# Kernel tuning notes

Measured on AMD Instinct MI355X. Metric: run time of the kernel, lower is better.

Reference implementation:

```python
import jax, jax.numpy as jnp
import numpy as np

INPUT_DIM = 1024
OUTPUT_DIM = 1024
NUM_SEGMENTS = 8
GRID_LO, GRID_HI = -1.0, 1.0


def setup_inputs() -> dict:
    key = jax.random.key(0)
    k1, k2 = jax.random.split(key)
    x = jax.random.normal(k1, (8, 2048, INPUT_DIM), dtype=jnp.float32)
    coeff = jax.random.normal(k2, (NUM_SEGMENTS + 1, OUTPUT_DIM, INPUT_DIM), dtype=jnp.float32) * 0.1
    bias = jnp.zeros((OUTPUT_DIM,), dtype=jnp.float32)
    return {"x": x, "coeff": coeff, "bias": bias}


def reference(x, coeff, bias):
    # x: (..., I); coeff: (G, O, I) with G = num_segments + 1; bias: (O,)
    batch_shape = x.shape[:-1]
    x_flat = x.reshape(-1, INPUT_DIM)                      # (B, I)
    grid = jnp.linspace(GRID_LO, GRID_HI, NUM_SEGMENTS + 1, dtype=x.dtype)  # (G,)
    h = (GRID_HI - GRID_LO) / NUM_SEGMENTS

    x_mean = jnp.mean(x_flat, axis=-1, keepdims=True)      # (B, 1)
    diff = x_mean - grid[None, :]                          # (B, G)
    w = jax.nn.relu(1.0 - jnp.abs(diff) / h)               # triangular hat weights
    w = w / (jnp.sum(w, axis=-1, keepdims=True) + 1e-8)    # (B, G)

    # Fused contraction order: avoid the (B, O, I) intermediate of the
    # original einsum chain; same math by associativity.
    t = jnp.einsum('bi,goi->bgo', x_flat, coeff)           # (B, G, O)
    out = jnp.einsum('bg,bgo->bo', w, t) + bias            # (B, O)
    return out.reshape(*batch_shape, OUTPUT_DIM)
```

## Files before the change

kernel.cpp:

```cpp
#include <hip/hip_runtime.h>
#include <math.h>

#define B_ROWS 16384
#define IDIM   1024
#define ODIM   1024
#define NGRID  9

#define RS_BLOCKS 1024
#define RS_ROWS   (B_ROWS / RS_BLOCKS)

#define GEMM_MSLOTS 80
#define GEMM_NT     8
#define GEMM_BLOCKS (GEMM_MSLOTS * GEMM_NT)

typedef __attribute__((ext_vector_type(8))) short frag8;
typedef __attribute__((ext_vector_type(4))) float f32x4;

typedef __attribute__((address_space(1))) void gvoid;
typedef __attribute__((address_space(3))) void lvoid;

__device__ __forceinline__ void async_cp16(const void* g, void* l) {
  __builtin_amdgcn_global_load_lds((gvoid*)(void*)g, (lvoid*)l, 16, 0, 0);
}

__device__ __forceinline__ unsigned short f2bf(float f) {
  union { float f; unsigned u; } v; v.f = f;
  unsigned u = v.u;
  u += 0x7fffu + ((u >> 16) & 1u);
  return (unsigned short)(u >> 16);
}

__device__ __forceinline__ void seg_weights(float m, int& sI, float& w0, float& w1) {
  float wsum = 0.f, wg[NGRID];
#pragma unroll
  for (int g = 0; g < NGRID; g++) {
    float gv = -1.f + 0.25f * (float)g;
    float t = 1.f - fabsf(m - gv) * 4.f;
    wg[g] = t > 0.f ? t : 0.f;
    wsum += wg[g];
  }
  int s = (int)floorf((m + 1.f) * 4.f);
  s = s < 0 ? 0 : (s > 7 ? 7 : s);
  float inv = 1.f / (wsum + 1e-8f);
  sI = s;
  w0 = wg[s] * inv;
  w1 = wg[s + 1] * inv;
}

__global__ void row_stats_fused(const float* __restrict__ x,
                                unsigned short* __restrict__ Xb,
                                float2* __restrict__ ws2,
                                int* __restrict__ seg_rows,
                                int* __restrict__ bucket_cnt) {
  __shared__ int lcnt[NGRID];
  __shared__ int base[NGRID];
  __shared__ int lrank[RS_ROWS];
  __shared__ int lseg[RS_ROWS];
  const int tid  = threadIdx.x;
  const int lane = tid & 63;
  const int wave = tid >> 6;
  if (tid < NGRID) lcnt[tid] = 0;
  __syncthreads();
  const int row0 = blockIdx.x * RS_ROWS;
#pragma unroll
  for (int it = 0; it < RS_ROWS / 4; ++it) {
    int r = it * 4 + wave;
    int b = row0 + r;
    const float4* xr = (const float4*)(x + (size_t)b * IDIM);
    ushort4* xw = (ushort4*)(Xb + (size_t)b * IDIM);
    float4 v[4];
    float s = 0.f;
#pragma unroll
    for (int j = 0; j < 4; j++) {
      v[j] = xr[lane + j * 64];
      s += v[j].x + v[j].y + v[j].z + v[j].w;
    }
#pragma unroll
    for (int j = 0; j < 4; j++) {
      ushort4 u;
      u.x = f2bf(v[j].x); u.y = f2bf(v[j].y); u.z = f2bf(v[j].z); u.w = f2bf(v[j].w);
      xw[lane + j * 64] = u;
    }
#pragma unroll
    for (int off = 32; off; off >>= 1) s += __shfl_down(s, off, 64);
    if (lane == 0) {
      float m = s * (1.0f / (float)IDIM);
      int sI; float w0, w1;
      seg_weights(m, sI, w0, w1);
      ws2[b] = make_float2(w0, w1);
      lseg[r] = sI;
      lrank[r] = atomicAdd(&lcnt[sI], 1);
    }
  }
  __syncthreads();
  if (tid < NGRID) base[tid] = lcnt[tid] ? atomicAdd(&bucket_cnt[tid], lcnt[tid]) : 0;
  __syncthreads();
  if (tid < RS_ROWS)
    seg_rows[lseg[tid] * B_ROWS + base[lseg[tid]] + lrank[tid]] = row0 + tid;
}

#define CV_BLKS_PER_PLANE (ODIM * IDIM / 4 / 256)
__global__ void cvt_coeff(const float* __restrict__ c, unsigned short* __restrict__ cb,
                          const int* __restrict__ bucket_cnt) {
  const int g  = blockIdx.x >> 10;
  const int cI = blockIdx.x & 1023;
  bool need = bucket_cnt[g] > 0;
  if (!need && g > 0) need = bucket_cnt[g - 1] > 0;
  if (!need) return;
  int i = (g * CV_BLKS_PER_PLANE + cI) * 256 + threadIdx.x;
  float4 v = ((const float4*)c)[i];
  ushort4 o;
  o.x = f2bf(v.x); o.y = f2bf(v.y); o.z = f2bf(v.z); o.w = f2bf(v.w);
  ((ushort4*)cb)[i] = o;
}

__global__ void __launch_bounds__(512, 2)
kan_gemm(const unsigned short* __restrict__ Xb,
         const unsigned short* __restrict__ Cb,
         const int* __restrict__ seg_rows,
         const int* __restrict__ bucket_cnt,
         const float2* __restrict__ ws2,
         const float* __restrict__ bias,
         float* __restrict__ out) {
  const int sub = blockIdx.x & 63;
  const int mt  = (blockIdx.x >> 6) * 8 + (sub & 7);
  const int nt  = sub >> 3;

  int seg = -1, lt = 0, cnt = 0;
  {
    int t0 = 0;
#pragma unroll
    for (int g = 0; g < NGRID; g++) {
      int c   = bucket_cnt[g];
      int ntg = (c + 255) >> 8;
      if (mt >= t0 && mt < t0 + ntg) { seg = g; lt = mt - t0; cnt = c; }
      t0 += ntg;
    }
  }
  if (seg < 0) return;
  const int rlim = cnt - lt * 256;
  const int* rows = seg_rows + seg * B_ROWS + lt * 256;

  __shared__ unsigned short As[2][256 * 64];
  __shared__ unsigned short Bs[2][256 * 64];
  __shared__ unsigned short scratch[512];

  const int tid  = threadIdx.x;
  const int lane = tid & 63;
  const int wave = tid >> 6;
  const int wm   = wave >> 2;
  const int wn   = wave & 3;
  const int colB0 = nt * 128;

  const int srow = lane >> 3;
  const int sc   = lane & 7;
  const int swc  = (((sc >> 2) ^ (srow & 1)) << 2) | ((sc & 3) ^ ((srow >> 1) & 3));
  const unsigned swkB = (unsigned)swc * 16;

  unsigned aOff[2][2], bOff[2][2];
#pragma unroll
  for (int h = 0; h < 2; h++)
#pragma unroll
    for (int i = 0; i < 2; i++) {
      int idx = h * 128 + wave * 16 + i * 8 + srow;
      int rid = rows[idx < rlim ? idx : rlim - 1];
      aOff[h][i] = (unsigned)rid * (IDIM * 2) + swkB;
      int realcol = wave * 16 + i * 8 + srow;
      bOff[h][i] = (unsigned)((seg + h) * ODIM + colB0 + realcol) * (IDIM * 2) + swkB;
    }

  int rofs[2];
#pragma unroll
  for (int kh = 0; kh < 2; kh++)
    rofs[kh] = ((((kh ^ (lane & 1)) << 2) | (((lane >> 4) & 3) ^ ((lane >> 1) & 3))) ) * 8;

  f32x4 acc[8][4] = {};
  frag8 af[8];
  frag8 bf[8];

#define STAGE_A(B, T, H) do {                                                  \
    const int tt_ = (T);                                                       \
    _Pragma("unroll")                                                          \
    for (int i_ = 0; i_ < 2; i_++) {                                           \
      unsigned short* dst_ = (tt_ < 16) ? &As[B][((H) * 128 + wave * 16 + i_ * 8) * 64] : scratch; \
      const char* src_ = (const char*)Xb + (tt_ < 16 ? (size_t)(aOff[H][i_] + (unsigned)tt_ * 128) : (size_t)swkB); \
      async_cp16(src_, dst_);                                                  \
    }                                                                          \
  } while (0)

#define STAGE_B(B, T, H) do {                                                  \
    const int tt_ = (T);                                                       \
    _Pragma("unroll")                                                          \
    for (int i_ = 0; i_ < 2; i_++) {                                           \
      unsigned short* dst_ = (tt_ < 16) ? &Bs[B][((H) * 128 + wave * 16 + i_ * 8) * 64] : scratch; \
      const char* src_ = (const char*)Cb + (tt_ < 16 ? (size_t)(bOff[H][i_] + (unsigned)tt_ * 128) : (size_t)swkB); \
      async_cp16(src_, dst_);                                                  \
    }                                                                          \
  } while (0)

#define LOAD_AF(B, MH) do {                                                    \
    _Pragma("unroll")                                                          \
    for (int mi_ = 0; mi_ < 4; mi_++)                                          \
      _Pragma("unroll")                                                        \
      for (int kh_ = 0; kh_ < 2; kh_++)                                        \
        af[mi_ * 2 + kh_] = *(const frag8*)&As[B][((MH) * 128 + wm * 64 + mi_ * 16 + (lane & 15)) * 64 + rofs[kh_]]; \
  } while (0)

#define LOAD_BF(B, NH) do {                                                    \
    _Pragma("unroll")                                                          \
    for (int ni_ = 0; ni_ < 2; ni_++)                                          \
      _Pragma("unroll")                                                        \
      for (int kh_ = 0; kh_ < 2; kh_++)                                        \
        bf[((NH) * 2 + ni_) * 2 + kh_] = *(const frag8*)&Bs[B][((NH) * 128 + wn * 32 + ni_ * 16 + (lane & 15)) * 64 + rofs[kh_]]; \
  } while (0)

#define MFMA_Q(MH, NH) do {                                                    \
    __builtin_amdgcn_s_setprio(1);                                             \
    _Pragma("unroll")                                                          \
    for (int mi_ = 0; mi_ < 4; mi_++)                                          \
      _Pragma("unroll")                                                        \
      for (int ni_ = 0; ni_ < 2; ni_++)                                        \
        _Pragma("unroll")                                                      \
        for (int kh_ = 0; kh_ < 2; kh_++)                                      \
          acc[(MH) * 4 + mi_][(NH) * 2 + ni_] = __builtin_amdgcn_mfma_f32_16x16x32_bf16( \
              af[mi_ * 2 + kh_], bf[((NH) * 2 + ni_) * 2 + kh_],               \
              acc[(MH) * 4 + mi_][(NH) * 2 + ni_], 0, 0, 0);                   \
    __builtin_amdgcn_s_setprio(0);                                             \
  } while (0)

#define VM10 asm volatile("s_waitcnt vmcnt(10)" ::: "memory")
#define BAR  asm volatile("s_barrier" ::: "memory")

  STAGE_A(0, 0, 0);
  STAGE_B(0, 0, 0);
  STAGE_B(0, 0, 1);
  STAGE_A(0, 0, 1);
  STAGE_A(1, 1, 0);
  STAGE_B(1, 1, 0);
  STAGE_B(1, 1, 1);
  VM10;
  BAR;

#pragma unroll 2
  for (int t = 0; t < 16; ++t) {
    const int buf  = t & 1;
    const int nbuf = buf ^ 1;
    LOAD_AF(buf, 0);
    LOAD_BF(buf, 0);
    STAGE_A(nbuf, t + 1, 1);
    VM10; BAR;
    MFMA_Q(0, 0);
    BAR;
    LOAD_BF(buf, 1);
    STAGE_A(buf, t + 2, 0);
    VM10; BAR;
    MFMA_Q(0, 1);
    BAR;
    LOAD_AF(buf, 1);
    STAGE_B(buf, t + 2, 0);
    BAR;
    MFMA_Q(1, 1);
    BAR;
    STAGE_B(buf, t + 2, 1);
    MFMA_Q(1, 0);
    VM10; BAR;
  }
#undef STAGE_A
#undef STAGE_B
#undef LOAD_AF
#undef LOAD_BF
#undef MFMA_Q

  int   col[2]; float bv[2];
#pragma unroll
  for (int nc = 0; nc < 2; nc++) {
    col[nc] = colB0 + wn * 32 + nc * 16 + (lane & 15);
    bv[nc]  = bias[col[nc]];
  }
#pragma unroll
  for (int mi = 0; mi < 8; mi++) {
    int irow = (mi >> 2) * 128 + wm * 64 + (mi & 3) * 16 + (lane >> 4) * 4;
#pragma unroll
    for (int r = 0; r < 4; r++) {
      int idx = irow + r;
      if (idx < rlim) {
        int orow = rows[idx];
        float2 w = ws2[orow];
        float* o = out + (size_t)orow * ODIM;
#pragma unroll
        for (int nc = 0; nc < 2; nc++)
          o[col[nc]] = w.x * acc[mi][nc][r] + w.y * acc[mi][2 + nc][r] + bv[nc];
      }
    }
  }
}

__global__ void fallback_kernel(const float* __restrict__ x, const float* __restrict__ coeff,
                                const float* __restrict__ bias, float* __restrict__ out) {
  int b = blockIdx.x;
  int tid = threadIdx.x;
  __shared__ float xs[IDIM];
  __shared__ float ps[4];
  __shared__ float mw[2];
  __shared__ int   ms;
  float4 v = ((const float4*)(x + (size_t)b * IDIM))[tid];
  ((float4*)xs)[tid] = v;
  float s = v.x + v.y + v.z + v.w;
#pragma unroll
  for (int off = 32; off; off >>= 1) s += __shfl_down(s, off, 64);
  if ((tid & 63) == 0) ps[tid >> 6] = s;
  __syncthreads();
  if (tid == 0) {
    float m = (ps[0] + ps[1] + ps[2] + ps[3]) * (1.0f / (float)IDIM);
    int sI; float w0, w1;
    seg_weights(m, sI, w0, w1);
    mw[0] = w0; mw[1] = w1; ms = sI;
  }
  __syncthreads();
  float w0 = mw[0], w1 = mw[1]; int sI = ms;
  for (int o = tid; o < ODIM; o += 256) {
    const float* c0 = coeff + ((size_t)sI * ODIM + o) * IDIM;
    const float* c1 = c0 + (size_t)ODIM * IDIM;
    float a0 = 0.f, a1 = 0.f;
    for (int i = 0; i < IDIM; i++) { a0 += xs[i] * c0[i]; a1 += xs[i] * c1[i]; }
    out[(size_t)b * ODIM + o] = w0 * a0 + w1 * a1 + bias[o];
  }
}

extern "C" void kernel_launch(void* const* d_in, const int* in_sizes, int n_in,
                              void* d_out, int out_size, void* d_ws, size_t ws_size,
                              hipStream_t stream) {
  const float* x     = (const float*)d_in[0];
  const float* coeff = (const float*)d_in[1];
  const float* bias  = (const float*)d_in[2];
  float* out = (float*)d_out;

  size_t szXb = (size_t)B_ROWS * IDIM * sizeof(unsigned short);
  size_t szCb = (size_t)NGRID * ODIM * IDIM * sizeof(unsigned short);
  size_t o0 = 0;
  unsigned short* Xb = (unsigned short*)((char*)d_ws + o0); o0 += szXb;
  unsigned short* Cb = (unsigned short*)((char*)d_ws + o0); o0 += szCb;
  float2* ws2 = (float2*)((char*)d_ws + o0); o0 += (size_t)B_ROWS * 8;
  int* seg_rows = (int*)((char*)d_ws + o0); o0 += (size_t)NGRID * B_ROWS * 4;
  int* bucket_cnt = (int*)((char*)d_ws + o0); o0 += 256;

  if (ws_size < o0) {
    fallback_kernel<<<B_ROWS, 256, 0, stream>>>(x, coeff, bias, out);
    return;
  }

  hipMemsetAsync(bucket_cnt, 0, NGRID * sizeof(int), stream);
  row_stats_fused<<<RS_BLOCKS, 256, 0, stream>>>(x, Xb, ws2, seg_rows, bucket_cnt);
  cvt_coeff<<<NGRID * CV_BLKS_PER_PLANE, 256, 0, stream>>>(coeff, Cb, bucket_cnt);
  kan_gemm<<<GEMM_BLOCKS, 512, 0, stream>>>(Xb, Cb, seg_rows, bucket_cnt, ws2, bias, out);
}
```

Measured before the change: 266.2 us.

## Restructure GEMM pipeline with manual double-buffer unroll, simpler swizzle, sorted weights

Unrolls the K loop by two with explicit buffer indices and reorders the async global-to-LDS stages. It adds lgkmcnt waits and sched_barriers, lowers the vmcnt threshold, and clamps out-of-range tiles to reload the last tile instead of using a scratch buffer. The LDS swizzle becomes a simple XOR on row index. Per-row hat weights are now written in segment-sorted order so the epilogue reads them contiguously. The aim is tighter overlap of loads with MFMA and less address arithmetic, at the cost of redundant loads on the tail iterations and more barriers.

```diff
diff --git a/kernel.cpp b/kernel.cpp
--- a/kernel.cpp
+++ b/kernel.cpp
@@ -49,13 +49,14 @@
 
 __global__ void row_stats_fused(const float* __restrict__ x,
                                 unsigned short* __restrict__ Xb,
-                                float2* __restrict__ ws2,
+                                float2* __restrict__ ws_s,
                                 int* __restrict__ seg_rows,
                                 int* __restrict__ bucket_cnt) {
   __shared__ int lcnt[NGRID];
   __shared__ int base[NGRID];
   __shared__ int lrank[RS_ROWS];
   __shared__ int lseg[RS_ROWS];
+  __shared__ float2 lws[RS_ROWS];
   const int tid  = threadIdx.x;
   const int lane = tid & 63;
   const int wave = tid >> 6;
@@ -87,7 +88,7 @@
       float m = s * (1.0f / (float)IDIM);
       int sI; float w0, w1;
       seg_weights(m, sI, w0, w1);
-      ws2[b] = make_float2(w0, w1);
+      lws[r] = make_float2(w0, w1);
       lseg[r] = sI;
       lrank[r] = atomicAdd(&lcnt[sI], 1);
     }
@@ -95,8 +96,11 @@
   __syncthreads();
   if (tid < NGRID) base[tid] = lcnt[tid] ? atomicAdd(&bucket_cnt[tid], lcnt[tid]) : 0;
   __syncthreads();
-  if (tid < RS_ROWS)
-    seg_rows[lseg[tid] * B_ROWS + base[lseg[tid]] + lrank[tid]] = row0 + tid;
+  if (tid < RS_ROWS) {
+    int p = lseg[tid] * B_ROWS + base[lseg[tid]] + lrank[tid];
+    seg_rows[p] = row0 + tid;
+    ws_s[p] = lws[tid];
+  }
 }
 
 #define CV_BLKS_PER_PLANE (ODIM * IDIM / 4 / 256)
@@ -119,7 +123,7 @@
          const unsigned short* __restrict__ Cb,
          const int* __restrict__ seg_rows,
          const int* __restrict__ bucket_cnt,
-         const float2* __restrict__ ws2,
+         const float2* __restrict__ ws_s,
          const float* __restrict__ bias,
          float* __restrict__ out) {
   const int sub = blockIdx.x & 63;
@@ -143,7 +147,6 @@
 
   __shared__ unsigned short As[2][256 * 64];
   __shared__ unsigned short Bs[2][256 * 64];
-  __shared__ unsigned short scratch[512];
 
   const int tid  = threadIdx.x;
   const int lane = tid & 63;
@@ -153,65 +156,62 @@
   const int colB0 = nt * 128;
 
   const int srow = lane >> 3;
-  const int sc   = lane & 7;
-  const int swc  = (((sc >> 2) ^ (srow & 1)) << 2) | ((sc & 3) ^ ((srow >> 1) & 3));
-  const unsigned swkB = (unsigned)swc * 16;
-
-  unsigned aOff[2][2], bOff[2][2];
+  const int sOff = ((lane & 7) ^ srow) * 8;
+
+  const unsigned short* gA[2][2];
+  const unsigned short* gB[2][2];
 #pragma unroll
   for (int h = 0; h < 2; h++)
 #pragma unroll
     for (int i = 0; i < 2; i++) {
       int idx = h * 128 + wave * 16 + i * 8 + srow;
       int rid = rows[idx < rlim ? idx : rlim - 1];
-      aOff[h][i] = (unsigned)rid * (IDIM * 2) + swkB;
+      gA[h][i] = Xb + (size_t)rid * IDIM + sOff;
       int realcol = wave * 16 + i * 8 + srow;
-      bOff[h][i] = (unsigned)((seg + h) * ODIM + colB0 + realcol) * (IDIM * 2) + swkB;
-    }
-
-  int rofs[2];
-#pragma unroll
-  for (int kh = 0; kh < 2; kh++)
-    rofs[kh] = ((((kh ^ (lane & 1)) << 2) | (((lane >> 4) & 3) ^ ((lane >> 1) & 3))) ) * 8;
+      gB[h][i] = Cb + ((size_t)((seg + h) * ODIM + colB0 + realcol)) * IDIM + sOff;
+    }
+
+  const int rsw0 = ((0 + ((lane >> 4) & 3)) ^ (lane & 7)) * 8;
+  const int rsw1 = ((4 + ((lane >> 4) & 3)) ^ (lane & 7)) * 8;
 
   f32x4 acc[8][4] = {};
   frag8 af[8];
   frag8 bf[8];
 
-#define STAGE_A(B, T, H) do {                                                  \
-    const int tt_ = (T);                                                       \
-    _Pragma("unroll")                                                          \
-    for (int i_ = 0; i_ < 2; i_++) {                                           \
-      unsigned short* dst_ = (tt_ < 16) ? &As[B][((H) * 128 + wave * 16 + i_ * 8) * 64] : scratch; \
-      const char* src_ = (const char*)Xb + (tt_ < 16 ? (size_t)(aOff[H][i_] + (unsigned)tt_ * 128) : (size_t)swkB); \
-      async_cp16(src_, dst_);                                                  \
+#define STAGE_A(BUF, T, H) do {                                                \
+    const int tt_ = (T) > 15 ? 15 : (T);                                       \
+    _Pragma("unroll")                                                          \
+    for (int i_ = 0; i_ < 2; i_++)                                             \
+      async_cp16(gA[H][i_] + tt_ * 64,                                         \
+                 &As[BUF][((H) * 128 + wave * 16 + i_ * 8) * 64]);             \
+    __builtin_amdgcn_sched_barrier(0);                                         \
+  } while (0)
+
+#define STAGE_B(BUF, T, H) do {                                                \
+    const int tt_ = (T) > 15 ? 15 : (T);                                       \
+    _Pragma("unroll")                                                          \
+    for (int i_ = 0; i_ < 2; i_++)                                             \
+      async_cp16(gB[H][i_] + tt_ * 64,                                         \
+                 &Bs[BUF][((H) * 128 + wave * 16 + i_ * 8) * 64]);             \
+    __builtin_amdgcn_sched_barrier(0);                                         \
+  } while (0)
+
+#define LOAD_AF(BUF, MH) do {                                                  \
+    _Pragma("unroll")                                                          \
+    for (int mi_ = 0; mi_ < 4; mi_++) {                                        \
+      const int r_ = ((MH) * 128 + wm * 64 + mi_ * 16 + (lane & 15)) * 64;     \
+      af[mi_ * 2 + 0] = *(const frag8*)&As[BUF][r_ + rsw0];                    \
+      af[mi_ * 2 + 1] = *(const frag8*)&As[BUF][r_ + rsw1];                    \
     }                                                                          \
   } while (0)
 
-#define STAGE_B(B, T, H) do {                                                  \
-    const int tt_ = (T);                                                       \
-    _Pragma("unroll")                                                          \
-    for (int i_ = 0; i_ < 2; i_++) {                                           \
-      unsigned short* dst_ = (tt_ < 16) ? &Bs[B][((H) * 128 + wave * 16 + i_ * 8) * 64] : scratch; \
-      const char* src_ = (const char*)Cb + (tt_ < 16 ? (size_t)(bOff[H][i_] + (unsigned)tt_ * 128) : (size_t)swkB); \
-      async_cp16(src_, dst_);                                                  \
+#define LOAD_BF(BUF, NH) do {                                                  \
+    _Pragma("unroll")                                                          \
+    for (int ni_ = 0; ni_ < 2; ni_++) {                                        \
+      const int r_ = ((NH) * 128 + wn * 32 + ni_ * 16 + (lane & 15)) * 64;     \
+      bf[((NH) * 2 + ni_) * 2 + 0] = *(const frag8*)&Bs[BUF][r_ + rsw0];       \
+      bf[((NH) * 2 + ni_) * 2 + 1] = *(const frag8*)&Bs[BUF][r_ + rsw1];       \
     }                                                                          \
-  } while (0)
-
-#define LOAD_AF(B, MH) do {                                                    \
-    _Pragma("unroll")                                                          \
-    for (int mi_ = 0; mi_ < 4; mi_++)                                          \
-      _Pragma("unroll")                                                        \
-      for (int kh_ = 0; kh_ < 2; kh_++)                                        \
-        af[mi_ * 2 + kh_] = *(const frag8*)&As[B][((MH) * 128 + wm * 64 + mi_ * 16 + (lane & 15)) * 64 + rofs[kh_]]; \
-  } while (0)
-
-#define LOAD_BF(B, NH) do {                                                    \
-    _Pragma("unroll")                                                          \
-    for (int ni_ = 0; ni_ < 2; ni_++)                                          \
-      _Pragma("unroll")                                                        \
-      for (int kh_ = 0; kh_ < 2; kh_++)                                        \
-        bf[((NH) * 2 + ni_) * 2 + kh_] = *(const frag8*)&Bs[B][((NH) * 128 + wn * 32 + ni_ * 16 + (lane & 15)) * 64 + rofs[kh_]]; \
   } while (0)
 
 #define MFMA_Q(MH, NH) do {                                                    \
@@ -222,55 +222,81 @@
       for (int ni_ = 0; ni_ < 2; ni_++)                                        \
         _Pragma("unroll")                                                      \
         for (int kh_ = 0; kh_ < 2; kh_++)                                      \
-          acc[(MH) * 4 + mi_][(NH) * 2 + ni_] = __builtin_amdgcn_mfma_f32_16x16x32_bf16( \
-              af[mi_ * 2 + kh_], bf[((NH) * 2 + ni_) * 2 + kh_],               \
-              acc[(MH) * 4 + mi_][(NH) * 2 + ni_], 0, 0, 0);                   \
+          acc[(MH) * 4 + mi_][(NH) * 2 + ni_] =                                \
+              __builtin_amdgcn_mfma_f32_16x16x32_bf16(                         \
+                  af[mi_ * 2 + kh_], bf[((NH) * 2 + ni_) * 2 + kh_],           \
+                  acc[(MH) * 4 + mi_][(NH) * 2 + ni_], 0, 0, 0);               \
     __builtin_amdgcn_s_setprio(0);                                             \
   } while (0)
 
-#define VM10 asm volatile("s_waitcnt vmcnt(10)" ::: "memory")
-#define BAR  asm volatile("s_barrier" ::: "memory")
+#define BAR   __builtin_amdgcn_s_barrier()
+#define LGKM0 do { asm volatile("s_waitcnt lgkmcnt(0)" ::: "memory");          \
+                   __builtin_amdgcn_sched_barrier(0); } while (0)
+#define VM6   do { asm volatile("s_waitcnt vmcnt(6)" ::: "memory");            \
+                   __builtin_amdgcn_sched_barrier(0); } while (0)
 
   STAGE_A(0, 0, 0);
   STAGE_B(0, 0, 0);
+  STAGE_A(0, 0, 1);
   STAGE_B(0, 0, 1);
-  STAGE_A(0, 0, 1);
   STAGE_A(1, 1, 0);
   STAGE_B(1, 1, 0);
-  STAGE_B(1, 1, 1);
-  VM10;
+  STAGE_A(1, 1, 1);
+  VM6;
   BAR;
 
-#pragma unroll 2
-  for (int t = 0; t < 16; ++t) {
-    const int buf  = t & 1;
-    const int nbuf = buf ^ 1;
-    LOAD_AF(buf, 0);
-    LOAD_BF(buf, 0);
-    STAGE_A(nbuf, t + 1, 1);
-    VM10; BAR;
+  for (int t = 0; t < 16; t += 2) {
+    LOAD_AF(0, 0); LOAD_BF(0, 0);
+    STAGE_B(1, t + 1, 1);
+    BAR; LGKM0;
     MFMA_Q(0, 0);
     BAR;
-    LOAD_BF(buf, 1);
-    STAGE_A(buf, t + 2, 0);
-    VM10; BAR;
+    LOAD_BF(0, 1);
+    STAGE_A(0, t + 2, 0);
+    BAR; LGKM0;
     MFMA_Q(0, 1);
     BAR;
-    LOAD_AF(buf, 1);
-    STAGE_B(buf, t + 2, 0);
-    BAR;
+    LOAD_AF(0, 1);
+    STAGE_B(0, t + 2, 0);
+    BAR; LGKM0;
     MFMA_Q(1, 1);
     BAR;
-    STAGE_B(buf, t + 2, 1);
+    STAGE_A(0, t + 2, 1);
+    BAR;
     MFMA_Q(1, 0);
-    VM10; BAR;
+    VM6;
+    BAR;
+    LOAD_AF(1, 0); LOAD_BF(1, 0);
+    STAGE_B(0, t + 2, 1);
+    BAR; LGKM0;
+    MFMA_Q(0, 0);
+    BAR;
+    LOAD_BF(1, 1);
+    STAGE_A(1, t + 3, 0);
+    BAR; LGKM0;
+    MFMA_Q(0, 1);
+    BAR;
+    LOAD_AF(1, 1);
+    STAGE_B(1, t + 3, 0);
+    BAR; LGKM0;
+    MFMA_Q(1, 1);
+    BAR;
+    STAGE_A(1, t + 3, 1);
+    BAR;
+    MFMA_Q(1, 0);
+    VM6;
+    BAR;
   }
 #undef STAGE_A
 #undef STAGE_B
 #undef LOAD_AF
 #undef LOAD_BF
 #undef MFMA_Q
-
+#undef BAR
+#undef LGKM0
+#undef VM6
+
+  const float2* wss = ws_s + seg * B_ROWS + lt * 256;
   int   col[2]; float bv[2];
 #pragma unroll
   for (int nc = 0; nc < 2; nc++) {
@@ -285,7 +311,7 @@
       int idx = irow + r;
       if (idx < rlim) {
         int orow = rows[idx];
-        float2 w = ws2[orow];
+        float2 w = wss[idx];
         float* o = out + (size_t)orow * ODIM;
 #pragma unroll
         for (int nc = 0; nc < 2; nc++)
@@ -340,7 +366,7 @@
   size_t o0 = 0;
   unsigned short* Xb = (unsigned short*)((char*)d_ws + o0); o0 += szXb;
   unsigned short* Cb = (unsigned short*)((char*)d_ws + o0); o0 += szCb;
-  float2* ws2 = (float2*)((char*)d_ws + o0); o0 += (size_t)B_ROWS * 8;
+  float2* ws_s = (float2*)((char*)d_ws + o0); o0 += (size_t)NGRID * B_ROWS * 8;
   int* seg_rows = (int*)((char*)d_ws + o0); o0 += (size_t)NGRID * B_ROWS * 4;
   int* bucket_cnt = (int*)((char*)d_ws + o0); o0 += 256;
 
@@ -350,7 +376,7 @@
   }
 
   hipMemsetAsync(bucket_cnt, 0, NGRID * sizeof(int), stream);
-  row_stats_fused<<<RS_BLOCKS, 256, 0, stream>>>(x, Xb, ws2, seg_rows, bucket_cnt);
+  row_stats_fused<<<RS_BLOCKS, 256, 0, stream>>>(x, Xb, ws_s, seg_rows, bucket_cnt);
   cvt_coeff<<<NGRID * CV_BLKS_PER_PLANE, 256, 0, stream>>>(coeff, Cb, bucket_cnt);
-  kan_gemm<<<GEMM_BLOCKS, 512, 0, stream>>>(Xb, Cb, seg_rows, bucket_cnt, ws2, bias, out);
-}
+  kan_gemm<<<GEMM_BLOCKS, 512, 0, stream>>>(Xb, Cb, seg_rows, bucket_cnt, ws_s, bias, out);
+}
```

Result: faster. 252.9 us (-5.0%).
